# Performance work log

Measured on AMD Instinct MI355X. Metric: run time of the kernel, lower is better.

Reference implementation:

```python
import jax, jax.numpy as jnp
import numpy as np

WORLD_SIZE = 8
RANK = 3              # simulated rank; exercises a non-trivial zig-zag mask
Q_HEAD = 32
KV_HEAD = 8
HEAD_DIM = 128
SEQLEN = 8192                         # max_seqlen_q == max_seqlen_k
Q_SHARD_LEN = SEQLEN // WORLD_SIZE    # 1024 tokens per rank
CHUNK = Q_SHARD_LEN // 2              # zig-zag chunk size (512)
GROUP = Q_HEAD // KV_HEAD             # GQA group size


def _zigzag_pos(r):
    # Global token positions owned by rank r under zig-zag partitioning:
    # sequence split into 2W chunks; rank r owns chunks r and (2W-1-r).
    a = jnp.arange(CHUNK) + r * CHUNK
    b = jnp.arange(CHUNK) + (2 * WORLD_SIZE - 1 - r) * CHUNK
    return jnp.concatenate([a, b])


def setup_inputs() -> dict:
    key = jax.random.key(0)
    k1, k2, k3 = jax.random.split(key, 3)
    q_shard = jax.random.normal(k1, (Q_SHARD_LEN, Q_HEAD, HEAD_DIM), jnp.float32)
    k_shard = jax.random.normal(k2, (WORLD_SIZE, SEQLEN // WORLD_SIZE, KV_HEAD, HEAD_DIM), jnp.float32)
    v_shard = jax.random.normal(k3, (WORLD_SIZE, SEQLEN // WORLD_SIZE, KV_HEAD, HEAD_DIM), jnp.float32)
    cu_seqlens_q = jnp.array([0, Q_SHARD_LEN], dtype=jnp.int32)
    cu_seqlens_k = jnp.array([0, SEQLEN], dtype=jnp.int32)
    return {"q_shard": q_shard, "k_shard": k_shard, "v_shard": v_shard,
            "cu_seqlens_q": cu_seqlens_q, "cu_seqlens_k": cu_seqlens_k}


def reference(q_shard, k_shard, v_shard, cu_seqlens_q, cu_seqlens_k):
    # All-gather of k/v shards across ranks == concat along sequence axis.
    k = k_shard.reshape(SEQLEN, KV_HEAD, HEAD_DIM)
    v = v_shard.reshape(SEQLEN, KV_HEAD, HEAD_DIM)

    # Global positions for this rank's queries and the gathered keys
    q_pos = _zigzag_pos(RANK)                                               # [Lq]
    k_pos = jnp.concatenate([_zigzag_pos(r) for r in range(WORLD_SIZE)])    # [Sk]

    scale = 1.0 / np.sqrt(HEAD_DIM).astype(np.float32)
    qg = q_shard.reshape(Q_SHARD_LEN, KV_HEAD, GROUP, HEAD_DIM)
    # scores: [Hkv, G, Lq, Sk]
    scores = jnp.einsum('qhgd,khd->hgqk', qg, k) * scale

    # Zig-zag causal mask on GLOBAL positions
    causal = q_pos[:, None] >= k_pos[None, :]                               # [Lq, Sk]
    scores = jnp.where(causal[None, None], scores, -jnp.inf)

    p = jax.nn.softmax(scores, axis=-1)
    out = jnp.einsum('hgqk,khd->qhgd', p, v)
    return out.reshape(Q_SHARD_LEN, Q_HEAD, HEAD_DIM)
```

## Files before the change

### kernel.cpp

```cpp
#include <hip/hip_runtime.h>
#include <hip/hip_bf16.h>

typedef __bf16 bf16x8 __attribute__((ext_vector_type(8)));
typedef float  f32x4  __attribute__((ext_vector_type(4)));

#define LQ   1024
#define HQ   32
#define HKV  8
#define GRP  4
#define DH   128
#define CHK  512
#define KB   32
#define RHN  (LQ * HQ)
#define NSPLIT 4
#define TILE_BYTES 8192
#define HKV_BYTES  (256 * TILE_BYTES)
#define QSCALE (0.08838834764831845f * 1.44269504088896341f)
#define MASKVAL (-3.0e38f)

typedef __attribute__((address_space(1))) const void gvoid_t;
typedef __attribute__((address_space(3))) void lvoid_t;
#define GLL(g, l) __builtin_amdgcn_global_load_lds((gvoid_t*)(g), (lvoid_t*)(l), 16, 0, 0)

__device__ __forceinline__ void load_qfrag(const float* __restrict__ qg,
                                           int qr0, int h, int l16, int lhi,
                                           bf16x8 (&qf)[4])
{
    const float* qp = qg + ((qr0 + l16) * HQ + h) * DH + lhi * 8;
    #pragma unroll
    for (int kb = 0; kb < 4; ++kb) {
        f32x4 t0 = *(const f32x4*)(qp + kb * 32);
        f32x4 t1 = *(const f32x4*)(qp + kb * 32 + 4);
        bf16x8 f;
        #pragma unroll
        for (int j = 0; j < 4; ++j) {
            f[j]     = (__bf16)(t0[j] * QSCALE);
            f[j + 4] = (__bf16)(t1[j] * QSCALE);
        }
        qf[kb] = f;
    }
}

__global__ __launch_bounds__(256)
void zz_prep(const float* __restrict__ kg, const float* __restrict__ vg,
             char* __restrict__ Kp, char* __restrict__ Vp)
{
    const int bid  = blockIdx.x;
    const int hkv  = bid & 7;
    const int tile = bid >> 3;
    const int tid  = threadIdx.x;
    char* ko = Kp + (size_t)hkv * HKV_BYTES + (size_t)tile * TILE_BYTES;
    char* vo = Vp + (size_t)hkv * HKV_BYTES + (size_t)tile * TILE_BYTES;

    #pragma unroll
    for (int p = 0; p < 2; ++p) {
        const int gid = tid + p * 256;
        const int key = gid >> 4;
        const int dbg = gid & 15;
        const float* src = kg + ((size_t)(tile * 32 + key) * HKV + hkv) * DH + dbg * 8;
        f32x4 t0 = *(const f32x4*)src;
        f32x4 t1 = *(const f32x4*)(src + 4);
        bf16x8 b;
        #pragma unroll
        for (int j = 0; j < 4; ++j) { b[j] = (__bf16)t0[j]; b[j + 4] = (__bf16)t1[j]; }
        *(bf16x8*)(ko + key * 256 + ((dbg * 16) ^ ((key & 7) << 4))) = b;
    }
    #pragma unroll
    for (int p = 0; p < 2; ++p) {
        const int gid = tid + p * 256;
        const int d   = gid & 127;
        const int kg2 = (tid >> 7) + p * 2;
        bf16x8 b;
        #pragma unroll
        for (int j = 0; j < 8; ++j)
            b[j] = (__bf16)vg[((size_t)(tile * 32 + kg2 * 8 + j) * HKV + hkv) * DH + d];
        *(bf16x8*)(vo + kg2 * 2048 + d * 16) = b;
    }
}

__global__ __launch_bounds__(256, 4)
void zz_part2(const float* __restrict__ qg, const char* __restrict__ Kp,
              const char* __restrict__ Vp,
              float* __restrict__ Op, float* __restrict__ mp, float* __restrict__ lp)
{
    __shared__ __align__(16) char lds[36864];
    const int bid = blockIdx.x;
    const int hkv = bid & 7;
    const int e   = bid >> 3;
    int half, part, q_tile;
    if (e < 32) { half = 0; part = 0; q_tile = e; }
    else { half = 1; part = (e - 32) >> 5; q_tile = 32 + ((e - 32) & 31); }

    const int tid  = threadIdx.x;
    const int w    = tid >> 6;
    const int lane = tid & 63;
    const int l16  = lane & 15;
    const int lhi  = lane >> 4;
    const int h    = hkv * GRP + w;
    const int qr0  = q_tile << 4;
    const int qrel0 = (q_tile & 31) << 4;

    bf16x8 qf[4];
    load_qfrag(qg, qr0, h, l16, lhi, qf);

    f32x4 acc[8];
    #pragma unroll
    for (int i = 0; i < 8; ++i) acc[i] = f32x4{0.f, 0.f, 0.f, 0.f};
    float m_r[4], l_r[4];
    #pragma unroll
    for (int r = 0; r < 4; ++r) { m_r[r] = -1e30f; l_r[r] = 0.f; }

    char* const pbase = lds + 32768 + w * 1024;

    unsigned fullmask; int diag_slot;
    if (half == 0) { fullmask = 0x0015u; diag_slot = 6; }
    else {
        fullmask = (part == 0) ? 0x0015u : (part == 1) ? 0x0340u
                 : (part == 2) ? 0x1C00u : 0xE000u;
        diag_slot = (part == 3) ? 7 : -1;
    }
    const int nd = (diag_slot >= 0) ? ((qrel0 >> 5) + 1) : 0;

    const char* kpg = Kp + (size_t)hkv * HKV_BYTES + w * 2048 + lane * 16;
    const char* vpg = Vp + (size_t)hkv * HKV_BYTES + w * 2048 + lane * 16;

    auto stage = [&](int gt, int b) {
        const char* kt = kpg + (size_t)gt * TILE_BYTES;
        const char* vt = vpg + (size_t)gt * TILE_BYTES;
        char* kd = lds + b * 16384 + w * 2048;
        GLL(kt, kd); GLL(kt + 1024, kd + 1024);
        char* vd = kd + 8192;
        GLL(vt, vd); GLL(vt + 1024, vd + 1024);
    };
    auto gt_of = [&](unsigned rem, int t) {
        return rem ? ((int)(__builtin_ctz(rem) << 4) + t) : (diag_slot * 16 + t);
    };
    auto adv = [](unsigned& rem, int& t) {
        ++t; if (rem && t == 16) { rem &= rem - 1; t = 0; }
    };

    const int ksw16 = (l16 & 7) << 4;
    const int vlane = lhi * 2048 + l16 * 16;

    unsigned remC = fullmask; int tC = 0;
    unsigned remN = remC;     int tN = 0; adv(remN, tN);
    stage(gt_of(remC, tC), 0);
    __syncthreads();
    int cur = 0;

    while (true) {
        const bool nv = (remN != 0) || (tN < nd);
        if (nv) stage(gt_of(remN, tN), cur ^ 1);

        char* kb_ = lds + cur * 16384;
        char* vb_ = kb_ + 8192;
        const bool masked = (remC == 0);
        const int  cbase  = masked ? (tC << 5) : 0;

        f32x4 s0 = f32x4{0.f, 0.f, 0.f, 0.f};
        f32x4 s1 = f32x4{0.f, 0.f, 0.f, 0.f};
        __builtin_amdgcn_s_setprio(1);
        #pragma unroll
        for (int kb = 0; kb < 4; ++kb) {
            const int dby = kb * 64 + lhi * 16;
            bf16x8 k0 = *(const bf16x8*)(kb_ + ((l16 * 256 + dby)        ^ ksw16));
            bf16x8 k1 = *(const bf16x8*)(kb_ + (((l16 + 16) * 256 + dby) ^ ksw16));
            s0 = __builtin_amdgcn_mfma_f32_16x16x32_bf16(qf[kb], k0, s0, 0, 0, 0);
            s1 = __builtin_amdgcn_mfma_f32_16x16x32_bf16(qf[kb], k1, s1, 0, 0, 0);
        }
        __builtin_amdgcn_s_setprio(0);

        if (masked) {
            #pragma unroll
            for (int r = 0; r < 4; ++r) {
                const int qrel = qrel0 + lhi * 4 + r;
                if (cbase + l16 > qrel)      s0[r] = MASKVAL;
                if (cbase + 16 + l16 > qrel) s1[r] = MASKVAL;
            }
        }

        float pmax[4];
        #pragma unroll
        for (int r = 0; r < 4; ++r) pmax[r] = fmaxf(s0[r], s1[r]);
        #pragma unroll
        for (int off = 1; off < 16; off <<= 1) {
            #pragma unroll
            for (int r = 0; r < 4; ++r)
                pmax[r] = fmaxf(pmax[r], __shfl_xor(pmax[r], off));
        }

        f32x4 p0, p1;
        float alpha[4], rsum[4];
        #pragma unroll
        for (int r = 0; r < 4; ++r) {
            const float mnew = fmaxf(m_r[r], pmax[r]);
            alpha[r] = exp2f(m_r[r] - mnew);
            m_r[r]   = mnew;
            p0[r] = exp2f(s0[r] - mnew);
            p1[r] = exp2f(s1[r] - mnew);
            rsum[r] = p0[r] + p1[r];
        }
        #pragma unroll
        for (int off = 1; off < 16; off <<= 1) {
            #pragma unroll
            for (int r = 0; r < 4; ++r)
                rsum[r] += __shfl_xor(rsum[r], off);
        }
        #pragma unroll
        for (int r = 0; r < 4; ++r) l_r[r] = l_r[r] * alpha[r] + rsum[r];
        #pragma unroll
        for (int nb = 0; nb < 8; ++nb) {
            #pragma unroll
            for (int r = 0; r < 4; ++r) acc[nb][r] *= alpha[r];
        }

        #pragma unroll
        for (int r = 0; r < 4; ++r) {
            const int rq  = lhi * 4 + r;
            const int rsw = (rq & 7) << 4;
            *(__bf16*)(pbase + ((rq * 64 + l16 * 2)        ^ rsw)) = (__bf16)p0[r];
            *(__bf16*)(pbase + ((rq * 64 + (l16 + 16) * 2) ^ rsw)) = (__bf16)p1[r];
        }
        bf16x8 pa = *(const bf16x8*)(pbase + ((l16 * 64 + lhi * 16) ^ ksw16));
        __builtin_amdgcn_s_setprio(1);
        #pragma unroll
        for (int nb = 0; nb < 8; ++nb) {
            bf16x8 vb = *(const bf16x8*)(vb_ + vlane + nb * 256);
            acc[nb] = __builtin_amdgcn_mfma_f32_16x16x32_bf16(pa, vb, acc[nb], 0, 0, 0);
        }
        __builtin_amdgcn_s_setprio(0);

        __syncthreads();
        if (!nv) break;
        cur ^= 1; remC = remN; tC = tN; adv(remN, tN);
    }

    float* op = Op + (size_t)part * (LQ * HQ * DH) + ((qr0 + lhi * 4) * HQ + h) * DH + l16;
    #pragma unroll
    for (int nb = 0; nb < 8; ++nb) {
        #pragma unroll
        for (int r = 0; r < 4; ++r)
            op[r * (HQ * DH) + nb * 16] = acc[nb][r];
    }
    if (l16 == 0) {
        #pragma unroll
        for (int r = 0; r < 4; ++r) {
            const int rh = (qr0 + lhi * 4 + r) * HQ + h;
            mp[part * RHN + rh] = m_r[r];
            lp[part * RHN + rh] = l_r[r];
            if (half == 0) {
                #pragma unroll
                for (int s = 1; s < NSPLIT; ++s) {
                    mp[s * RHN + rh] = -1e30f;
                    lp[s * RHN + rh] = 0.f;
                }
            }
        }
    }
}

__global__ __launch_bounds__(256)
void zz_combine(const float* __restrict__ Op, const float* __restrict__ mp,
                const float* __restrict__ lp, float* __restrict__ outg)
{
    const int flat = blockIdx.x * 256 + threadIdx.x;
    const int rh = flat >> 5;
    const int d4 = (flat & 31) << 2;
    const float m0 = mp[rh], m1 = mp[RHN + rh], m2 = mp[2 * RHN + rh], m3 = mp[3 * RHN + rh];
    const float M  = fmaxf(fmaxf(m0, m1), fmaxf(m2, m3));
    const float w0 = exp2f(m0 - M), w1 = exp2f(m1 - M), w2 = exp2f(m2 - M), w3 = exp2f(m3 - M);
    const float den = w0 * lp[rh] + w1 * lp[RHN + rh] + w2 * lp[2 * RHN + rh] + w3 * lp[3 * RHN + rh];
    const size_t base = (size_t)rh * DH + d4;
    f32x4 a0 = *(const f32x4*)(Op + base);
    f32x4 a1 = *(const f32x4*)(Op + (size_t)LQ * HQ * DH + base);
    f32x4 a2 = *(const f32x4*)(Op + (size_t)2 * LQ * HQ * DH + base);
    f32x4 a3 = *(const f32x4*)(Op + (size_t)3 * LQ * HQ * DH + base);
    f32x4 num = w0 * a0 + w1 * a1 + w2 * a2 + w3 * a3;
    const float inv = 1.0f / den;
    *(f32x4*)(outg + base) = num * inv;
}

__device__ __forceinline__ void attn_tile_f32(
    char* __restrict__ lds, char* __restrict__ pbase,
    const float* __restrict__ kg, const float* __restrict__ vg,
    int hkv, int krow, int cbase, bool masked,
    int tid, int l16, int lhi, int qrel0,
    const bf16x8 (&qf)[4], f32x4 (&acc)[8], float (&m_r)[4], float (&l_r)[4])
{
    __syncthreads();
    {
        const int key = tid >> 3;
        const int d0  = (tid & 7) << 4;
        const float* kp = kg + ((krow + key) * HKV + hkv) * DH + d0;
        const float* vp = vg + ((krow + key) * HKV + hkv) * DH + d0;
        f32x4 a0 = *(const f32x4*)(kp);
        f32x4 a1 = *(const f32x4*)(kp + 4);
        f32x4 a2 = *(const f32x4*)(kp + 8);
        f32x4 a3 = *(const f32x4*)(kp + 12);
        bf16x8 b0, b1;
        #pragma unroll
        for (int j = 0; j < 4; ++j) {
            b0[j] = (__bf16)a0[j]; b0[j + 4] = (__bf16)a1[j];
            b1[j] = (__bf16)a2[j]; b1[j + 4] = (__bf16)a3[j];
        }
        const int kbyte = key * 256 + d0 * 2;
        const int ksw   = (key & 7) << 4;
        *(bf16x8*)(lds + ((kbyte)      ^ ksw)) = b0;
        *(bf16x8*)(lds + ((kbyte + 16) ^ ksw)) = b1;

        f32x4 c0 = *(const f32x4*)(vp);
        f32x4 c1 = *(const f32x4*)(vp + 4);
        f32x4 c2 = *(const f32x4*)(vp + 8);
        f32x4 c3 = *(const f32x4*)(vp + 12);
        #pragma unroll
        for (int i = 0; i < 16; ++i) {
            float fv = (i < 4) ? c0[i] : (i < 8) ? c1[i - 4]
                     : (i < 12) ? c2[i - 8] : c3[i - 12];
            const int d = d0 + i;
            const int vsw = ((d & 7) ^ ((d >> 4) & 7)) << 4;
            const int vbyte = (d * 64 + key * 2) ^ vsw;
            *(__bf16*)(lds + 8192 + vbyte) = (__bf16)fv;
        }
    }
    __syncthreads();

    f32x4 s0 = f32x4{0.f, 0.f, 0.f, 0.f};
    f32x4 s1 = f32x4{0.f, 0.f, 0.f, 0.f};
    #pragma unroll
    for (int kb = 0; kb < 4; ++kb) {
        const int dby = (kb * 32 + lhi * 8) * 2;
        bf16x8 k0 = *(const bf16x8*)(lds + ((l16 * 256 + dby)        ^ ((l16 & 7) << 4)));
        bf16x8 k1 = *(const bf16x8*)(lds + (((l16 + 16) * 256 + dby) ^ ((l16 & 7) << 4)));
        s0 = __builtin_amdgcn_mfma_f32_16x16x32_bf16(qf[kb], k0, s0, 0, 0, 0);
        s1 = __builtin_amdgcn_mfma_f32_16x16x32_bf16(qf[kb], k1, s1, 0, 0, 0);
    }
    if (masked) {
        #pragma unroll
        for (int r = 0; r < 4; ++r) {
            const int qrel = qrel0 + lhi * 4 + r;
            if (cbase + l16 > qrel)      s0[r] = MASKVAL;
            if (cbase + 16 + l16 > qrel) s1[r] = MASKVAL;
        }
    }
    float pmax[4];
    #pragma unroll
    for (int r = 0; r < 4; ++r) pmax[r] = fmaxf(s0[r], s1[r]);
    #pragma unroll
    for (int off = 1; off < 16; off <<= 1) {
        #pragma unroll
        for (int r = 0; r < 4; ++r)
            pmax[r] = fmaxf(pmax[r], __shfl_xor(pmax[r], off));
    }
    f32x4 p0, p1;
    float alpha[4], rsum[4];
    #pragma unroll
    for (int r = 0; r < 4; ++r) {
        const float mnew = fmaxf(m_r[r], pmax[r]);
        alpha[r] = exp2f(m_r[r] - mnew);
        m_r[r]   = mnew;
        p0[r] = exp2f(s0[r] - mnew);
        p1[r] = exp2f(s1[r] - mnew);
        rsum[r] = p0[r] + p1[r];
    }
    #pragma unroll
    for (int off = 1; off < 16; off <<= 1) {
        #pragma unroll
        for (int r = 0; r < 4; ++r)
            rsum[r] += __shfl_xor(rsum[r], off);
    }
    #pragma unroll
    for (int r = 0; r < 4; ++r) l_r[r] = l_r[r] * alpha[r] + rsum[r];
    #pragma unroll
    for (int nb = 0; nb < 8; ++nb) {
        #pragma unroll
        for (int r = 0; r < 4; ++r) acc[nb][r] *= alpha[r];
    }
    #pragma unroll
    for (int r = 0; r < 4; ++r) {
        const int rq  = lhi * 4 + r;
        const int rsw = (rq & 7) << 4;
        *(__bf16*)(pbase + ((rq * 64 + l16 * 2)        ^ rsw)) = (__bf16)p0[r];
        *(__bf16*)(pbase + ((rq * 64 + (l16 + 16) * 2) ^ rsw)) = (__bf16)p1[r];
    }
    bf16x8 pa = *(const bf16x8*)(pbase + ((l16 * 64 + lhi * 16) ^ ((l16 & 7) << 4)));
    #pragma unroll
    for (int nb = 0; nb < 8; ++nb) {
        const int d = nb * 16 + l16;
        const int vsw = ((d & 7) ^ (nb & 7)) << 4;
        bf16x8 vb = *(const bf16x8*)(lds + 8192 + ((d * 64 + lhi * 16) ^ vsw));
        acc[nb] = __builtin_amdgcn_mfma_f32_16x16x32_bf16(pa, vb, acc[nb], 0, 0, 0);
    }
}

__global__ __launch_bounds__(256, 2)
void zz_attn_part_old(const float* __restrict__ qg, const float* __restrict__ kg,
                      const float* __restrict__ vg,
                      float* __restrict__ Op, float* __restrict__ mp, float* __restrict__ lp)
{
    __shared__ __align__(16) char lds[20480];
    const int bid = blockIdx.x;
    int half, part, q_tile, hkv;
    if (bid < 256) { half = 0; part = 0; q_tile = bid & 31; hkv = bid >> 5; }
    else { const int e = bid - 256; half = 1; part = e & 3;
           q_tile = 32 + ((e >> 2) & 31); hkv = e >> 7; }
    const int tid  = threadIdx.x;
    const int w    = tid >> 6;
    const int lane = tid & 63;
    const int l16  = lane & 15;
    const int lhi  = lane >> 4;
    const int h    = hkv * GRP + w;
    const int qr0  = q_tile << 4;
    const int qrel0 = (q_tile & 31) << 4;

    bf16x8 qf[4];
    load_qfrag(qg, qr0, h, l16, lhi, qf);
    f32x4 acc[8];
    #pragma unroll
    for (int i = 0; i < 8; ++i) acc[i] = f32x4{0.f, 0.f, 0.f, 0.f};
    float m_r[4], l_r[4];
    #pragma unroll
    for (int r = 0; r < 4; ++r) { m_r[r] = -1e30f; l_r[r] = 0.f; }
    char* const pbase = lds + 16384 + w * 1024;

    unsigned fullmask; int diag_slot;
    if (half == 0) { fullmask = 0x0015u; diag_slot = 6; }
    else {
        fullmask = (part == 0) ? 0x0015u : (part == 1) ? 0x0340u
                 : (part == 2) ? 0x1C00u : 0xE000u;
        diag_slot = (part == 3) ? 7 : -1;
    }
    #pragma unroll 1
    for (int s = 0; s < 16; ++s) {
        if (!((fullmask >> s) & 1)) continue;
        #pragma unroll 1
        for (int t = 0; t < 16; ++t)
            attn_tile_f32(lds, pbase, kg, vg, hkv, s * CHK + t * KB, 0, false,
                          tid, l16, lhi, qrel0, qf, acc, m_r, l_r);
    }
    if (diag_slot >= 0) {
        const int nd = (qrel0 >> 5) + 1;
        #pragma unroll 1
        for (int t = 0; t < nd; ++t)
            attn_tile_f32(lds, pbase, kg, vg, hkv, diag_slot * CHK + t * KB, t * KB, true,
                          tid, l16, lhi, qrel0, qf, acc, m_r, l_r);
    }
    float* op = Op + (size_t)part * (LQ * HQ * DH) + ((qr0 + lhi * 4) * HQ + h) * DH + l16;
    #pragma unroll
    for (int nb = 0; nb < 8; ++nb) {
        #pragma unroll
        for (int r = 0; r < 4; ++r)
            op[r * (HQ * DH) + nb * 16] = acc[nb][r];
    }
    if (l16 == 0) {
        #pragma unroll
        for (int r = 0; r < 4; ++r) {
            const int rh = (qr0 + lhi * 4 + r) * HQ + h;
            mp[part * RHN + rh] = m_r[r];
            lp[part * RHN + rh] = l_r[r];
            if (half == 0) {
                #pragma unroll
                for (int s = 1; s < NSPLIT; ++s) {
                    mp[s * RHN + rh] = -1e30f;
                    lp[s * RHN + rh] = 0.f;
                }
            }
        }
    }
}

extern "C" void kernel_launch(void* const* d_in, const int* in_sizes, int n_in,
                              void* d_out, int out_size, void* d_ws, size_t ws_size,
                              hipStream_t stream)
{
    (void)in_sizes; (void)n_in; (void)out_size;
    const float* q = (const float*)d_in[0];
    const float* k = (const float*)d_in[1];
    const float* v = (const float*)d_in[2];
    float* out = (float*)d_out;

    const size_t sz_op = (size_t)NSPLIT * LQ * HQ * DH * 4;
    const size_t sz_ml = (size_t)NSPLIT * RHN * 4;
    const size_t sz_kv = (size_t)HKV * HKV_BYTES;
    const size_t need_split = sz_op + 2 * sz_ml;
    const size_t need_full  = need_split + 2 * sz_kv;

    float* Op = (float*)d_ws;
    float* mp = (float*)((char*)d_ws + sz_op);
    float* lp = (float*)((char*)d_ws + sz_op + sz_ml);

    if (ws_size >= need_full) {
        char* Kp = (char*)d_ws + need_split;
        char* Vp = Kp + sz_kv;
        hipLaunchKernelGGL(zz_prep,  dim3(2048), dim3(256), 0, stream, k, v, Kp, Vp);
        hipLaunchKernelGGL(zz_part2, dim3(1280), dim3(256), 0, stream, q, Kp, Vp, Op, mp, lp);
        hipLaunchKernelGGL(zz_combine, dim3((RHN * DH / 4) / 256), dim3(256), 0, stream,
                           Op, mp, lp, out);
    } else {
        hipLaunchKernelGGL(zz_attn_part_old, dim3(1280), dim3(256), 0, stream, q, k, v, Op, mp, lp);
        hipLaunchKernelGGL(zz_combine, dim3((RHN * DH / 4) / 256), dim3(256), 0, stream,
                           Op, mp, lp, out);
    }
}
```

Measured before the change: 383.9 us.

## Share K/V tiles across two query tiles per block and defer softmax rescale

Each block now runs 512 threads covering two adjacent 16-row query tiles for the same KV head, so every staged K/V tile in LDS serves eight waves instead of four. This halves the grid and the per-wave global-to-LDS loads, cutting redundant K/V traffic. It also adds a lazy online-softmax rescale: when no row's max grows by more than a threshold, the old max is kept and the alpha rescale of the accumulators is skipped. The P-buffer swizzle is changed to avoid bank conflicts with the larger layout. The risks are lower occupancy from the larger blocks and a shared loop count set by the longer diagonal range, since nd now depends on the tile pair.

Result: slower. 1.510 ms (+293.4%).

```diff
diff --git a/kernel.cpp b/kernel.cpp
--- a/kernel.cpp
+++ b/kernel.cpp
@@ -17,6 +17,7 @@
 #define HKV_BYTES  (256 * TILE_BYTES)
 #define QSCALE (0.08838834764831845f * 1.44269504088896341f)
 #define MASKVAL (-3.0e38f)
+#define DEFER_THR 8.0f
 
 typedef __attribute__((address_space(1))) const void gvoid_t;
 typedef __attribute__((address_space(3))) void lvoid_t;
@@ -78,25 +79,28 @@
     }
 }
 
-__global__ __launch_bounds__(256, 4)
+__global__ __launch_bounds__(512, 8)
 void zz_part2(const float* __restrict__ qg, const char* __restrict__ Kp,
               const char* __restrict__ Vp,
               float* __restrict__ Op, float* __restrict__ mp, float* __restrict__ lp)
 {
-    __shared__ __align__(16) char lds[36864];
+    __shared__ __align__(16) char lds[40960];
     const int bid = blockIdx.x;
     const int hkv = bid & 7;
     const int e   = bid >> 3;
-    int half, part, q_tile;
-    if (e < 32) { half = 0; part = 0; q_tile = e; }
-    else { half = 1; part = (e - 32) >> 5; q_tile = 32 + ((e - 32) & 31); }
+    int half, part, qbase;
+    if (e < 16) { half = 0; part = 0; qbase = e * 2; }
+    else { const int f = e - 16; half = 1; part = f >> 4; qbase = 32 + (f & 15) * 2; }
 
     const int tid  = threadIdx.x;
     const int w    = tid >> 6;
+    const int hw   = w & 3;
+    const int qsel = w >> 2;
     const int lane = tid & 63;
     const int l16  = lane & 15;
     const int lhi  = lane >> 4;
-    const int h    = hkv * GRP + w;
+    const int h    = hkv * GRP + hw;
+    const int q_tile = qbase + qsel;
     const int qr0  = q_tile << 4;
     const int qrel0 = (q_tile & 31) << 4;
 
@@ -119,18 +123,15 @@
                  : (part == 2) ? 0x1C00u : 0xE000u;
         diag_slot = (part == 3) ? 7 : -1;
     }
-    const int nd = (diag_slot >= 0) ? ((qrel0 >> 5) + 1) : 0;
-
-    const char* kpg = Kp + (size_t)hkv * HKV_BYTES + w * 2048 + lane * 16;
-    const char* vpg = Vp + (size_t)hkv * HKV_BYTES + w * 2048 + lane * 16;
+    const int nd = (diag_slot >= 0) ? (((q_tile & 31) >> 1) + 1) : 0;
+
+    const char* kpg = Kp + (size_t)hkv * HKV_BYTES + w * 1024 + lane * 16;
+    const char* vpg = Vp + (size_t)hkv * HKV_BYTES + w * 1024 + lane * 16;
 
     auto stage = [&](int gt, int b) {
-        const char* kt = kpg + (size_t)gt * TILE_BYTES;
-        const char* vt = vpg + (size_t)gt * TILE_BYTES;
-        char* kd = lds + b * 16384 + w * 2048;
-        GLL(kt, kd); GLL(kt + 1024, kd + 1024);
-        char* vd = kd + 8192;
-        GLL(vt, vd); GLL(vt + 1024, vd + 1024);
+        char* dst = lds + b * 16384 + w * 1024;
+        GLL(kpg + (size_t)gt * TILE_BYTES, dst);
+        GLL(vpg + (size_t)gt * TILE_BYTES, dst + 8192);
     };
     auto gt_of = [&](unsigned rem, int t) {
         return rem ? ((int)(__builtin_ctz(rem) << 4) + t) : (diag_slot * 16 + t);
@@ -140,6 +141,7 @@
     };
 
     const int ksw16 = (l16 & 7) << 4;
+    const int psw   = ((l16 & 7) << 4) ^ ((l16 & 8) << 2);
     const int vlane = lhi * 2048 + l16 * 16;
 
     unsigned remC = fullmask; int tC = 0;
@@ -189,39 +191,61 @@
                 pmax[r] = fmaxf(pmax[r], __shfl_xor(pmax[r], off));
         }
 
+        bool ok = true;
+        #pragma unroll
+        for (int r = 0; r < 4; ++r) ok = ok && (pmax[r] - m_r[r] <= DEFER_THR);
+
         f32x4 p0, p1;
-        float alpha[4], rsum[4];
-        #pragma unroll
-        for (int r = 0; r < 4; ++r) {
-            const float mnew = fmaxf(m_r[r], pmax[r]);
-            alpha[r] = exp2f(m_r[r] - mnew);
-            m_r[r]   = mnew;
-            p0[r] = exp2f(s0[r] - mnew);
-            p1[r] = exp2f(s1[r] - mnew);
-            rsum[r] = p0[r] + p1[r];
-        }
-        #pragma unroll
-        for (int off = 1; off < 16; off <<= 1) {
-            #pragma unroll
-            for (int r = 0; r < 4; ++r)
-                rsum[r] += __shfl_xor(rsum[r], off);
-        }
-        #pragma unroll
-        for (int r = 0; r < 4; ++r) l_r[r] = l_r[r] * alpha[r] + rsum[r];
-        #pragma unroll
-        for (int nb = 0; nb < 8; ++nb) {
-            #pragma unroll
-            for (int r = 0; r < 4; ++r) acc[nb][r] *= alpha[r];
+        float rsum[4];
+        if (__all(ok)) {
+            #pragma unroll
+            for (int r = 0; r < 4; ++r) {
+                p0[r] = exp2f(s0[r] - m_r[r]);
+                p1[r] = exp2f(s1[r] - m_r[r]);
+                rsum[r] = p0[r] + p1[r];
+            }
+            #pragma unroll
+            for (int off = 1; off < 16; off <<= 1) {
+                #pragma unroll
+                for (int r = 0; r < 4; ++r)
+                    rsum[r] += __shfl_xor(rsum[r], off);
+            }
+            #pragma unroll
+            for (int r = 0; r < 4; ++r) l_r[r] += rsum[r];
+        } else {
+            float alpha[4];
+            #pragma unroll
+            for (int r = 0; r < 4; ++r) {
+                const float mnew = fmaxf(m_r[r], pmax[r]);
+                alpha[r] = exp2f(m_r[r] - mnew);
+                m_r[r]   = mnew;
+                p0[r] = exp2f(s0[r] - mnew);
+                p1[r] = exp2f(s1[r] - mnew);
+                rsum[r] = p0[r] + p1[r];
+            }
+            #pragma unroll
+            for (int off = 1; off < 16; off <<= 1) {
+                #pragma unroll
+                for (int r = 0; r < 4; ++r)
+                    rsum[r] += __shfl_xor(rsum[r], off);
+            }
+            #pragma unroll
+            for (int r = 0; r < 4; ++r) l_r[r] = l_r[r] * alpha[r] + rsum[r];
+            #pragma unroll
+            for (int nb = 0; nb < 8; ++nb) {
+                #pragma unroll
+                for (int r = 0; r < 4; ++r) acc[nb][r] *= alpha[r];
+            }
         }
 
         #pragma unroll
         for (int r = 0; r < 4; ++r) {
             const int rq  = lhi * 4 + r;
-            const int rsw = (rq & 7) << 4;
+            const int rsw = ((rq & 7) << 4) ^ ((rq & 8) << 2);
             *(__bf16*)(pbase + ((rq * 64 + l16 * 2)        ^ rsw)) = (__bf16)p0[r];
             *(__bf16*)(pbase + ((rq * 64 + (l16 + 16) * 2) ^ rsw)) = (__bf16)p1[r];
         }
-        bf16x8 pa = *(const bf16x8*)(pbase + ((l16 * 64 + lhi * 16) ^ ksw16));
+        bf16x8 pa = *(const bf16x8*)(pbase + ((l16 * 64 + lhi * 16) ^ psw));
         __builtin_amdgcn_s_setprio(1);
         #pragma unroll
         for (int nb = 0; nb < 8; ++nb) {
@@ -492,7 +516,7 @@
         char* Kp = (char*)d_ws + need_split;
         char* Vp = Kp + sz_kv;
         hipLaunchKernelGGL(zz_prep,  dim3(2048), dim3(256), 0, stream, k, v, Kp, Vp);
-        hipLaunchKernelGGL(zz_part2, dim3(1280), dim3(256), 0, stream, q, Kp, Vp, Op, mp, lp);
+        hipLaunchKernelGGL(zz_part2, dim3(640), dim3(512), 0, stream, q, Kp, Vp, Op, mp, lp);
         hipLaunchKernelGGL(zz_combine, dim3((RHN * DH / 4) / 256), dim3(256), 0, stream,
                            Op, mp, lp, out);
     } else {
```
